# Performance work log

Hardware: AMD Instinct MI355X
Metric: run time of the kernel (lower is better)

Reference implementation:

```python
import jax, jax.numpy as jnp
import numpy as np

APREC = 8   # activation fractional bits
PPREC = 8   # parameter fractional bits
IWIDTH = 3  # integer width -> clamp to [-2**IWIDTH, 2**IWIDTH - 1]

QMAX = 2.0 ** IWIDTH - 1.0
QMIN = -(2.0 ** IWIDTH)


def quant(v, prec):
    # round to 2**-prec grid (torch.round and jnp.round both round-half-to-even)
    s = 2.0 ** prec
    return jnp.round(v * s) / s


def round_max(v):
    # the relu-chain in the source is exactly a clamp to [QMIN, QMAX]
    return jnp.clip(v, QMIN, QMAX)


def fixed_point_conv(x, w, b):
    """Quantized 'conv': each elementwise product w[j,m,p,q]*x[b,m,k+p,l+q] is
    rounded to the activation grid and clamped BEFORE summation, then bias added.
    x: [B,Cin,H,W], w: [Cout,Cin,K,K], b: [Cout].
    Loop is over the KxK fixed kernel offsets (25), fully vectorized over B/Cout/Cin/space."""
    w = quant(w, PPREC)
    b = quant(b, PPREC)
    K = w.shape[2]
    Ho = x.shape[2] - K + 1
    Wo = x.shape[3] - K + 1
    out = jnp.zeros((x.shape[0], w.shape[0], Ho, Wo), dtype=x.dtype)
    for p in range(K):
        for q in range(K):
            # [B, Cout, Cin, Ho, Wo]
            prod = x[:, None, :, p:p + Ho, q:q + Wo] * w[None, :, :, p, q, None, None]
            prod = round_max(quant(prod, APREC))
            out = out + prod.sum(axis=2)
    return out + b[None, :, None, None]


def fixed_point_fc(x, w, b):
    # x: [B, in], w: [out, in], b: [out]
    w = round_max(quant(w, PPREC))
    b = round_max(quant(b, PPREC))
    x = round_max(quant(x, APREC))
    out = x @ w.T + b[None, :]
    out = round_max(out)
    return quant(out, APREC)


def max_pool2(x):
    return jax.lax.reduce_window(x, -jnp.inf, jax.lax.max,
                                 (1, 1, 2, 2), (1, 1, 2, 2), 'VALID')


def setup_inputs() -> dict:
    key = jax.random.key(0)
    ks = jax.random.split(key, 9)
    B = 2048
    return {
        'x': jax.random.normal(ks[0], (B, 1, 28, 28), jnp.float32),
        'conv1_w': jax.random.normal(ks[1], (10, 1, 5, 5), jnp.float32) * 0.2,
        'conv1_b': jax.random.normal(ks[2], (10,), jnp.float32) * 0.1,
        'conv2_w': jax.random.normal(ks[3], (20, 10, 5, 5), jnp.float32) * 0.1,
        'conv2_b': jax.random.normal(ks[4], (20,), jnp.float32) * 0.1,
        'fc1_w': jax.random.normal(ks[5], (50, 320), jnp.float32) * 0.05,
        'fc1_b': jax.random.normal(ks[6], (50,), jnp.float32) * 0.05,
        'fc2_w': jax.random.normal(ks[7], (10, 50), jnp.float32) * 0.1,
        'fc2_b': jax.random.normal(ks[8], (10,), jnp.float32) * 0.1,
    }


def reference(x, conv1_w, conv1_b, conv2_w, conv2_b, fc1_w, fc1_b, fc2_w, fc2_b):
    x = quant(x, APREC)
    conv1_input = x
    x = fixed_point_conv(x, conv1_w, conv1_b)          # [B,10,24,24]
    x = quant(x, APREC)
    conv1_output = x
    x = jax.nn.relu(max_pool2(x))                      # [B,10,12,12]
    x = quant(x, APREC)
    conv2_input = x
    x = fixed_point_conv(x, conv2_w, conv2_b)          # [B,20,8,8]
    x = quant(x, APREC)
    conv2_output = x
    # Dropout2d / F.dropout are identity in eval mode
    x = jax.nn.relu(max_pool2(x))                      # [B,20,4,4]
    x = x.reshape(-1, 320)
    x = quant(x, APREC)
    fc1_input = x
    x = fixed_point_fc(x, fc1_w, fc1_b)                # [B,50]
    x = quant(x, APREC)
    fc1_output = x
    x = jax.nn.relu(x)
    x = quant(x, APREC)
    fc2_input = x
    x = fixed_point_fc(x, fc2_w, fc2_b)                # [B,10]
    x = quant(x, APREC)
    fc2_output = x
    logp = jax.nn.log_softmax(x, axis=1)
    return (logp, conv1_input, conv1_output, conv2_input, conv2_output,
            fc1_input, fc1_output, fc2_input, fc2_output)
```

## Files before the change

### kernel.cpp

```cpp
#include <hip/hip_runtime.h>
#include <math.h>


#define NB 2048

#define OFF_LOGP   0
#define OFF_C1IN   (OFF_LOGP  + NB*10)
#define OFF_C1OUT  (OFF_C1IN  + NB*784)
#define OFF_C2IN   (OFF_C1OUT + NB*5760)
#define OFF_C2OUT  (OFF_C2IN  + NB*1440)
#define OFF_FC1IN  (OFF_C2OUT + NB*1280)
#define OFF_FC1OUT (OFF_FC1IN + NB*320)
#define OFF_FC2IN  (OFF_FC1OUT+ NB*50)
#define OFF_FC2OUT (OFF_FC2IN + NB*50)

__device__ __forceinline__ float clamp8(float v) {
    return __builtin_amdgcn_fmed3f(v, -8.0f, 7.0f);
}

__global__ __launch_bounds__(256, 3)
void k1_conv1(const float* __restrict__ x,
              const float* __restrict__ cw1, const float* __restrict__ cb1,
              float* __restrict__ out)
{
    __shared__ float s_w1[125];
    __shared__ float s_b1[5];
    __shared__ __align__(16) float s_x[784];

    const int t    = threadIdx.x;
    const int img  = blockIdx.x >> 1;
    const int half = blockIdx.x & 1;

    if (t < 125) s_w1[t] = rintf(cw1[half * 125 + t] * 256.0f);
    if (t < 5)   s_b1[t] = rintf(cb1[half * 5 + t] * 256.0f);

    const float* xg = x + (size_t)img * 784;
    float* c1in_g = out + OFF_C1IN + (size_t)img * 784;
    for (int i = t; i < 784; i += 256) {
        float v = rintf(xg[i] * 256.0f) * (1.0f / 256.0f);
        s_x[i] = v;
        if (half == 0) c1in_g[i] = v;
    }
    __syncthreads();

    if (t < 240) {
        const int co_l = t / 48;
        const int co   = half * 5 + co_l;
        const int r    = t % 48;
        const int i    = r >> 1;
        const int jh   = r & 1;

        float acc[12];
        #pragma unroll
        for (int j = 0; j < 12; j++) acc[j] = 0.0f;

        #pragma unroll
        for (int p = 0; p < 5; p++) {
            float xr[16];
            const float* row = &s_x[(i + p) * 28 + 12 * jh];
            #pragma unroll
            for (int k = 0; k < 4; k++) {
                float4 v4 = *(const float4*)(row + 4 * k);
                xr[4*k] = v4.x; xr[4*k+1] = v4.y; xr[4*k+2] = v4.z; xr[4*k+3] = v4.w;
            }
            #pragma unroll
            for (int q = 0; q < 5; q++) {
                float w = s_w1[co_l * 25 + p * 5 + q];
                #pragma unroll
                for (int j = 0; j < 12; j++) {
                    acc[j] += rintf(xr[q + j] * w);
                }
            }
        }
        const float b = s_b1[co_l];
        float v[12];
        #pragma unroll
        for (int j = 0; j < 12; j++) v[j] = (acc[j] + b) * (1.0f / 256.0f);

        float* gdst = out + OFF_C1OUT + (size_t)img * 5760 + co * 576 + i * 24 + 12 * jh;
        #pragma unroll
        for (int k = 0; k < 3; k++) {
            float4 st = { v[4*k], v[4*k+1], v[4*k+2], v[4*k+3] };
            *(float4*)(gdst + 4 * k) = st;
        }

        float m[6];
        #pragma unroll
        for (int j2 = 0; j2 < 6; j2++) m[j2] = fmaxf(v[2*j2], v[2*j2+1]);
        float pm[6];
        #pragma unroll
        for (int j2 = 0; j2 < 6; j2++) pm[j2] = __shfl_xor(m[j2], 2);

        if ((i & 1) == 0) {
            float pr[6];
            #pragma unroll
            for (int j2 = 0; j2 < 6; j2++)
                pr[j2] = fmaxf(fmaxf(m[j2], pm[j2]), 0.0f);
            float* g = out + OFF_C2IN + (size_t)img * 1440 + co * 144 + (i >> 1) * 12 + 6 * jh;
            #pragma unroll
            for (int k = 0; k < 3; k++) {
                float2 st = { pr[2*k], pr[2*k+1] };
                *(float2*)(g + 2 * k) = st;
            }
        }
    }
}

__global__ __launch_bounds__(320, 2)
void k2_rest(const float* __restrict__ cw2, const float* __restrict__ cb2,
             const float* __restrict__ fw1, const float* __restrict__ fb1,
             const float* __restrict__ fw2, const float* __restrict__ fb2,
             float* __restrict__ out)
{
    __shared__ __align__(16) float s_w2[5600];
    __shared__ float s_b2[20];
    __shared__ __align__(16) float s_p1[1440];
    __shared__ float s_p2[320];
    __shared__ float s_fc2in[50];
    __shared__ float s_fc2out[10];

    const int t   = threadIdx.x;
    const int img = blockIdx.x;

    for (int idx = t; idx < 5000; idx += 320) {
        int cc = idx / 25, q = idx % 25;
        s_w2[cc * 28 + q] = rintf(cw2[idx] * 256.0f);
    }
    if (t < 20) s_b2[t] = rintf(cb2[t] * 256.0f);

    const float* p1g = out + OFF_C2IN + (size_t)img * 1440;
    for (int i = t; i < 1440; i += 320) s_p1[i] = p1g[i];
    __syncthreads();

    const int co = t >> 4;
    const int i  = (t >> 1) & 7;
    const int jh = t & 1;

    float acc[4] = {0.f, 0.f, 0.f, 0.f};
    for (int ci = 0; ci < 10; ci++) {
        float wr_[28];
        const float* wb = s_w2 + (co * 10 + ci) * 28;
        #pragma unroll
        for (int k = 0; k < 7; k++) {
            float4 v4 = *(const float4*)(wb + 4 * k);
            wr_[4*k] = v4.x; wr_[4*k+1] = v4.y; wr_[4*k+2] = v4.z; wr_[4*k+3] = v4.w;
        }
        const float* xb = s_p1 + ci * 144 + jh * 4;
        #pragma unroll
        for (int p = 0; p < 5; p++) {
            const float* row = xb + (i + p) * 12;
            float4 a4 = *(const float4*)(row);
            float4 b4 = *(const float4*)(row + 4);
            float xr[8] = { a4.x, a4.y, a4.z, a4.w, b4.x, b4.y, b4.z, b4.w };
            #pragma unroll
            for (int q = 0; q < 5; q++) {
                float w = wr_[p * 5 + q];
                #pragma unroll
                for (int j = 0; j < 4; j++) {
                    acc[j] += rintf(xr[q + j] * w);
                }
            }
        }
    }
    const float b2 = s_b2[co];
    float v[4];
    #pragma unroll
    for (int j = 0; j < 4; j++) v[j] = (acc[j] + b2) * (1.0f / 256.0f);

    {
        float4 st = { v[0], v[1], v[2], v[3] };
        *(float4*)(out + OFF_C2OUT + (size_t)img * 1280 + co * 64 + i * 8 + jh * 4) = st;
    }

    float m0 = fmaxf(v[0], v[1]);
    float m1 = fmaxf(v[2], v[3]);
    float pm0 = __shfl_xor(m0, 2);
    float pm1 = __shfl_xor(m1, 2);
    if ((i & 1) == 0) {
        float r0 = fmaxf(fmaxf(m0, pm0), 0.0f);
        float r1 = fmaxf(fmaxf(m1, pm1), 0.0f);
        int o = co * 16 + (i >> 1) * 4 + jh * 2;
        out[OFF_FC1IN + (size_t)img * 320 + o]     = r0;
        out[OFF_FC1IN + (size_t)img * 320 + o + 1] = r1;
        s_p2[o]     = clamp8(r0);
        s_p2[o + 1] = clamp8(r1);
    }
    __syncthreads();

    float* s_fcp = s_p1;
    if (t < 250) {
        const int j = t / 5, c = t % 5;
        const float* wr = fw1 + j * 320 + c * 64;
        const float* xr = s_p2 + c * 64;
        float s = 0.0f;
        #pragma unroll 8
        for (int k = 0; k < 64; k++) {
            float wq = clamp8(rintf(wr[k] * 256.0f) * (1.0f / 256.0f));
            s = fmaf(xr[k], wq, s);
        }
        s_fcp[t] = s;
    }
    __syncthreads();

    if (t < 50) {
        float acc1 = clamp8(rintf(fb1[t] * 256.0f) * (1.0f / 256.0f));
        #pragma unroll
        for (int c = 0; c < 5; c++) acc1 += s_fcp[t * 5 + c];
        float o1 = rintf(clamp8(acc1) * 256.0f) * (1.0f / 256.0f);
        out[OFF_FC1OUT + (size_t)img * 50 + t] = o1;
        float r = fmaxf(o1, 0.0f);
        out[OFF_FC2IN + (size_t)img * 50 + t] = r;
        s_fc2in[t] = clamp8(r);
    }
    __syncthreads();

    if (t < 10) {
        float acc2 = clamp8(rintf(fb2[t] * 256.0f) * (1.0f / 256.0f));
        const float* wr = fw2 + t * 50;
        for (int k = 0; k < 50; k++) {
            float wq = clamp8(rintf(wr[k] * 256.0f) * (1.0f / 256.0f));
            acc2 = fmaf(s_fc2in[k], wq, acc2);
        }
        float o2 = rintf(clamp8(acc2) * 256.0f) * (1.0f / 256.0f);
        out[OFF_FC2OUT + (size_t)img * 10 + t] = o2;
        s_fc2out[t] = o2;
    }
    __syncthreads();

    if (t == 0) {
        float m = s_fc2out[0];
        for (int k = 1; k < 10; k++) m = fmaxf(m, s_fc2out[k]);
        float ssum = 0.0f;
        for (int k = 0; k < 10; k++) ssum += expf(s_fc2out[k] - m);
        float lse = m + logf(ssum);
        for (int k = 0; k < 10; k++)
            out[OFF_LOGP + (size_t)img * 10 + k] = s_fc2out[k] - lse;
    }
}

extern "C" void kernel_launch(void* const* d_in, const int* in_sizes, int n_in,
                              void* d_out, int out_size, void* d_ws, size_t ws_size,
                              hipStream_t stream) {
    const float* x   = (const float*)d_in[0];
    const float* cw1 = (const float*)d_in[1];
    const float* cb1 = (const float*)d_in[2];
    const float* cw2 = (const float*)d_in[3];
    const float* cb2 = (const float*)d_in[4];
    const float* fw1 = (const float*)d_in[5];
    const float* fb1 = (const float*)d_in[6];
    const float* fw2 = (const float*)d_in[7];
    const float* fb2 = (const float*)d_in[8];
    float* o = (float*)d_out;

    k1_conv1<<<2 * NB, 256, 0, stream>>>(x, cw1, cb1, o);
    k2_rest <<<NB, 320, 0, stream>>>(cw2, cb2, fw1, fb1, fw2, fb2, o);
}
```

Before: 191.7 us.

## Fuse conv1 and rest into one kernel processing four images per block

Merges the two kernels into a single kernel in which each 320-thread block handles four images. Conv1 results stay in LDS for conv2, so the global round-trip of the pooled activations disappears, and the conv2 weights are loaded once per four images instead of once per image. Conv2 is re-tiled so each thread computes a 4x4 output patch with register-cached inputs, and the fc1 weights are read as float4. In exchange the grid has only 512 blocks with about 59KB of LDS each, which reduces occupancy and parallelism.

```diff
diff --git a/kernel.cpp b/kernel.cpp
--- a/kernel.cpp
+++ b/kernel.cpp
@@ -14,41 +14,73 @@
 #define OFF_FC2IN  (OFF_FC1OUT+ NB*50)
 #define OFF_FC2OUT (OFF_FC2IN + NB*50)
 
+#define W1_OFF  0
+#define B1_OFF  280
+#define B2_OFF  290
+#define W2_OFF  312
+#define X_OFF   5912
+#define P1_OFF  9048
+#define LDS_FLOATS 14808
+#define P2_OFF   X_OFF
+#define FC2IN_OFF (X_OFF + 1280)
+#define FC2OUT_OFF (X_OFF + 1488)
+
 __device__ __forceinline__ float clamp8(float v) {
     return __builtin_amdgcn_fmed3f(v, -8.0f, 7.0f);
 }
 
-__global__ __launch_bounds__(256, 3)
-void k1_conv1(const float* __restrict__ x,
-              const float* __restrict__ cw1, const float* __restrict__ cb1,
-              float* __restrict__ out)
+__global__ __launch_bounds__(320, 2)
+void net_fused(const float* __restrict__ x,
+               const float* __restrict__ cw1, const float* __restrict__ cb1,
+               const float* __restrict__ cw2, const float* __restrict__ cb2,
+               const float* __restrict__ fw1, const float* __restrict__ fb1,
+               const float* __restrict__ fw2, const float* __restrict__ fb2,
+               float* __restrict__ out)
 {
-    __shared__ float s_w1[125];
-    __shared__ float s_b1[5];
-    __shared__ __align__(16) float s_x[784];
+    __shared__ __align__(16) float lds[LDS_FLOATS];
 
     const int t    = threadIdx.x;
-    const int img  = blockIdx.x >> 1;
-    const int half = blockIdx.x & 1;
-
-    if (t < 125) s_w1[t] = rintf(cw1[half * 125 + t] * 256.0f);
-    if (t < 5)   s_b1[t] = rintf(cb1[half * 5 + t] * 256.0f);
-
-    const float* xg = x + (size_t)img * 784;
-    float* c1in_g = out + OFF_C1IN + (size_t)img * 784;
-    for (int i = t; i < 784; i += 256) {
-        float v = rintf(xg[i] * 256.0f) * (1.0f / 256.0f);
-        s_x[i] = v;
-        if (half == 0) c1in_g[i] = v;
-    }
-    __syncthreads();
-
-    if (t < 240) {
-        const int co_l = t / 48;
-        const int co   = half * 5 + co_l;
-        const int r    = t % 48;
-        const int i    = r >> 1;
-        const int jh   = r & 1;
+    const int img0 = blockIdx.x * 4;
+
+    if (t < 250) lds[W1_OFF + (t / 25) * 28 + (t % 25)] = rintf(cw1[t] * 256.0f);
+    if (t < 10)  lds[B1_OFF + t] = rintf(cb1[t] * 256.0f);
+    if (t < 20)  lds[B2_OFF + t] = rintf(cb2[t] * 256.0f);
+    for (int f = t; f < 5000; f += 320) {
+        int cc = f / 25, q = f % 25;
+        lds[W2_OFF + cc * 28 + q] = rintf(cw2[f] * 256.0f);
+    }
+
+    {
+        const float* xg = x + (size_t)img0 * 784;
+        float* g = out + OFF_C1IN + (size_t)img0 * 784;
+        for (int f = t; f < 3136; f += 320) {
+            float v = rintf(xg[f] * 256.0f) * (1.0f / 256.0f);
+            lds[X_OFF + f] = v;
+            g[f] = v;
+        }
+    }
+    __syncthreads();
+
+    #pragma unroll 1
+    for (int iter = 0; iter < 6; iter++) {
+        const int T     = iter * 320 + t;
+        const int img_l = T / 480;
+        const int rem   = T % 480;
+        const int co    = rem / 48;
+        const int r     = rem % 48;
+        const int i     = r >> 1;
+        const int jh    = r & 1;
+        const int img   = img0 + img_l;
+
+        float wreg[28];
+        {
+            const float* wb = lds + W1_OFF + co * 28;
+            #pragma unroll
+            for (int k = 0; k < 7; k++) {
+                float4 v4 = *(const float4*)(wb + 4 * k);
+                wreg[4*k] = v4.x; wreg[4*k+1] = v4.y; wreg[4*k+2] = v4.z; wreg[4*k+3] = v4.w;
+            }
+        }
 
         float acc[12];
         #pragma unroll
@@ -57,7 +89,7 @@
         #pragma unroll
         for (int p = 0; p < 5; p++) {
             float xr[16];
-            const float* row = &s_x[(i + p) * 28 + 12 * jh];
+            const float* row = lds + X_OFF + img_l * 784 + (i + p) * 28 + 12 * jh;
             #pragma unroll
             for (int k = 0; k < 4; k++) {
                 float4 v4 = *(const float4*)(row + 4 * k);
@@ -65,14 +97,13 @@
             }
             #pragma unroll
             for (int q = 0; q < 5; q++) {
-                float w = s_w1[co_l * 25 + p * 5 + q];
+                float w = wreg[p * 5 + q];
                 #pragma unroll
-                for (int j = 0; j < 12; j++) {
+                for (int j = 0; j < 12; j++)
                     acc[j] += rintf(xr[q + j] * w);
-                }
-            }
-        }
-        const float b = s_b1[co_l];
+            }
+        }
+        const float b = lds[B1_OFF + co];
         float v[12];
         #pragma unroll
         for (int j = 0; j < 12; j++) v[j] = (acc[j] + b) * (1.0f / 256.0f);
@@ -96,145 +127,158 @@
             #pragma unroll
             for (int j2 = 0; j2 < 6; j2++)
                 pr[j2] = fmaxf(fmaxf(m[j2], pm[j2]), 0.0f);
-            float* g = out + OFF_C2IN + (size_t)img * 1440 + co * 144 + (i >> 1) * 12 + 6 * jh;
+            const int o = co * 144 + (i >> 1) * 12 + 6 * jh;
+            float* g = out + OFF_C2IN + (size_t)img * 1440 + o;
+            float* s = lds + P1_OFF + img_l * 1440 + o;
             #pragma unroll
             for (int k = 0; k < 3; k++) {
                 float2 st = { pr[2*k], pr[2*k+1] };
                 *(float2*)(g + 2 * k) = st;
-            }
-        }
-    }
-}
-
-__global__ __launch_bounds__(320, 2)
-void k2_rest(const float* __restrict__ cw2, const float* __restrict__ cb2,
-             const float* __restrict__ fw1, const float* __restrict__ fb1,
-             const float* __restrict__ fw2, const float* __restrict__ fb2,
-             float* __restrict__ out)
-{
-    __shared__ __align__(16) float s_w2[5600];
-    __shared__ float s_b2[20];
-    __shared__ __align__(16) float s_p1[1440];
-    __shared__ float s_p2[320];
-    __shared__ float s_fc2in[50];
-    __shared__ float s_fc2out[10];
-
-    const int t   = threadIdx.x;
-    const int img = blockIdx.x;
-
-    for (int idx = t; idx < 5000; idx += 320) {
-        int cc = idx / 25, q = idx % 25;
-        s_w2[cc * 28 + q] = rintf(cw2[idx] * 256.0f);
-    }
-    if (t < 20) s_b2[t] = rintf(cb2[t] * 256.0f);
-
-    const float* p1g = out + OFF_C2IN + (size_t)img * 1440;
-    for (int i = t; i < 1440; i += 320) s_p1[i] = p1g[i];
-    __syncthreads();
-
-    const int co = t >> 4;
-    const int i  = (t >> 1) & 7;
-    const int jh = t & 1;
-
-    float acc[4] = {0.f, 0.f, 0.f, 0.f};
-    for (int ci = 0; ci < 10; ci++) {
-        float wr_[28];
-        const float* wb = s_w2 + (co * 10 + ci) * 28;
-        #pragma unroll
-        for (int k = 0; k < 7; k++) {
-            float4 v4 = *(const float4*)(wb + 4 * k);
-            wr_[4*k] = v4.x; wr_[4*k+1] = v4.y; wr_[4*k+2] = v4.z; wr_[4*k+3] = v4.w;
-        }
-        const float* xb = s_p1 + ci * 144 + jh * 4;
-        #pragma unroll
-        for (int p = 0; p < 5; p++) {
-            const float* row = xb + (i + p) * 12;
-            float4 a4 = *(const float4*)(row);
-            float4 b4 = *(const float4*)(row + 4);
-            float xr[8] = { a4.x, a4.y, a4.z, a4.w, b4.x, b4.y, b4.z, b4.w };
-            #pragma unroll
-            for (int q = 0; q < 5; q++) {
-                float w = wr_[p * 5 + q];
+                s[2*k] = pr[2*k]; s[2*k+1] = pr[2*k+1];
+            }
+        }
+    }
+    __syncthreads();
+
+    {
+        const int img_l = t / 80;
+        const int rt    = t % 80;
+        const int co    = rt >> 2;
+        const int ih    = (rt >> 1) & 1;
+        const int jh    = rt & 1;
+        const int img   = img0 + img_l;
+
+        float acc[16];
+        #pragma unroll
+        for (int j = 0; j < 16; j++) acc[j] = 0.0f;
+
+        const float* wbase  = lds + W2_OFF + co * 280;
+        const float* xibase = lds + P1_OFF + img_l * 1440 + jh * 4;
+        #pragma unroll 1
+        for (int ci = 0; ci < 10; ci++) {
+            float wreg[28];
+            {
+                const float* wb = wbase + ci * 28;
                 #pragma unroll
-                for (int j = 0; j < 4; j++) {
-                    acc[j] += rintf(xr[q + j] * w);
+                for (int k = 0; k < 7; k++) {
+                    float4 v4 = *(const float4*)(wb + 4 * k);
+                    wreg[4*k] = v4.x; wreg[4*k+1] = v4.y; wreg[4*k+2] = v4.z; wreg[4*k+3] = v4.w;
                 }
             }
-        }
-    }
-    const float b2 = s_b2[co];
-    float v[4];
-    #pragma unroll
-    for (int j = 0; j < 4; j++) v[j] = (acc[j] + b2) * (1.0f / 256.0f);
-
-    {
-        float4 st = { v[0], v[1], v[2], v[3] };
-        *(float4*)(out + OFF_C2OUT + (size_t)img * 1280 + co * 64 + i * 8 + jh * 4) = st;
-    }
-
-    float m0 = fmaxf(v[0], v[1]);
-    float m1 = fmaxf(v[2], v[3]);
-    float pm0 = __shfl_xor(m0, 2);
-    float pm1 = __shfl_xor(m1, 2);
-    if ((i & 1) == 0) {
-        float r0 = fmaxf(fmaxf(m0, pm0), 0.0f);
-        float r1 = fmaxf(fmaxf(m1, pm1), 0.0f);
-        int o = co * 16 + (i >> 1) * 4 + jh * 2;
-        out[OFF_FC1IN + (size_t)img * 320 + o]     = r0;
-        out[OFF_FC1IN + (size_t)img * 320 + o + 1] = r1;
-        s_p2[o]     = clamp8(r0);
-        s_p2[o + 1] = clamp8(r1);
-    }
-    __syncthreads();
-
-    float* s_fcp = s_p1;
-    if (t < 250) {
-        const int j = t / 5, c = t % 5;
+            float xr[64];
+            const float* xb = xibase + ci * 144 + ih * 48;
+            #pragma unroll
+            for (int rr = 0; rr < 8; rr++) {
+                float4 a4 = *(const float4*)(xb + rr * 12);
+                float4 b4 = *(const float4*)(xb + rr * 12 + 4);
+                xr[rr*8+0] = a4.x; xr[rr*8+1] = a4.y; xr[rr*8+2] = a4.z; xr[rr*8+3] = a4.w;
+                xr[rr*8+4] = b4.x; xr[rr*8+5] = b4.y; xr[rr*8+6] = b4.z; xr[rr*8+7] = b4.w;
+            }
+            #pragma unroll
+            for (int p = 0; p < 5; p++) {
+                #pragma unroll
+                for (int q = 0; q < 5; q++) {
+                    float w = wreg[p * 5 + q];
+                    #pragma unroll
+                    for (int rr = 0; rr < 4; rr++) {
+                        #pragma unroll
+                        for (int cc = 0; cc < 4; cc++)
+                            acc[rr*4+cc] += rintf(xr[(rr+p)*8 + q + cc] * w);
+                    }
+                }
+            }
+        }
+        const float b2 = lds[B2_OFF + co];
+        float v[16];
+        #pragma unroll
+        for (int j = 0; j < 16; j++) v[j] = (acc[j] + b2) * (1.0f / 256.0f);
+
+        float* gdst = out + OFF_C2OUT + (size_t)img * 1280 + co * 64 + ih * 32 + jh * 4;
+        #pragma unroll
+        for (int rr = 0; rr < 4; rr++) {
+            float4 st = { v[rr*4+0], v[rr*4+1], v[rr*4+2], v[rr*4+3] };
+            *(float4*)(gdst + rr * 8) = st;
+        }
+
+        #pragma unroll
+        for (int a = 0; a < 2; a++) {
+            #pragma unroll
+            for (int bb = 0; bb < 2; bb++) {
+                float pm = fmaxf(fmaxf(v[(2*a)*4 + 2*bb], v[(2*a)*4 + 2*bb + 1]),
+                                 fmaxf(v[(2*a+1)*4 + 2*bb], v[(2*a+1)*4 + 2*bb + 1]));
+                pm = fmaxf(pm, 0.0f);
+                const int o = co * 16 + (ih * 2 + a) * 4 + (jh * 2 + bb);
+                out[OFF_FC1IN + (size_t)img * 320 + o] = pm;
+                lds[P2_OFF + img_l * 320 + o] = clamp8(pm);
+            }
+        }
+    }
+    __syncthreads();
+
+    float* s_fcp = lds + P1_OFF;
+    #pragma unroll 1
+    for (int T = t; T < 1000; T += 320) {
+        const int img_l = T / 250;
+        const int rem   = T % 250;
+        const int j     = rem / 5;
+        const int c     = rem % 5;
         const float* wr = fw1 + j * 320 + c * 64;
-        const float* xr = s_p2 + c * 64;
+        const float* xr = lds + P2_OFF + img_l * 320 + c * 64;
         float s = 0.0f;
-        #pragma unroll 8
-        for (int k = 0; k < 64; k++) {
-            float wq = clamp8(rintf(wr[k] * 256.0f) * (1.0f / 256.0f));
-            s = fmaf(xr[k], wq, s);
-        }
-        s_fcp[t] = s;
-    }
-    __syncthreads();
-
-    if (t < 50) {
-        float acc1 = clamp8(rintf(fb1[t] * 256.0f) * (1.0f / 256.0f));
-        #pragma unroll
-        for (int c = 0; c < 5; c++) acc1 += s_fcp[t * 5 + c];
+        #pragma unroll
+        for (int k4 = 0; k4 < 16; k4++) {
+            float4 w4 = *(const float4*)(wr + 4 * k4);
+            s = fmaf(xr[4*k4+0], clamp8(rintf(w4.x * 256.0f) * (1.0f / 256.0f)), s);
+            s = fmaf(xr[4*k4+1], clamp8(rintf(w4.y * 256.0f) * (1.0f / 256.0f)), s);
+            s = fmaf(xr[4*k4+2], clamp8(rintf(w4.z * 256.0f) * (1.0f / 256.0f)), s);
+            s = fmaf(xr[4*k4+3], clamp8(rintf(w4.w * 256.0f) * (1.0f / 256.0f)), s);
+        }
+        s_fcp[T] = s;
+    }
+    __syncthreads();
+
+    if (t < 200) {
+        const int img_l = t / 50;
+        const int j     = t % 50;
+        const int img   = img0 + img_l;
+        float acc1 = clamp8(rintf(fb1[j] * 256.0f) * (1.0f / 256.0f));
+        #pragma unroll
+        for (int c = 0; c < 5; c++) acc1 += s_fcp[img_l * 250 + j * 5 + c];
         float o1 = rintf(clamp8(acc1) * 256.0f) * (1.0f / 256.0f);
-        out[OFF_FC1OUT + (size_t)img * 50 + t] = o1;
+        out[OFF_FC1OUT + (size_t)img * 50 + j] = o1;
         float r = fmaxf(o1, 0.0f);
-        out[OFF_FC2IN + (size_t)img * 50 + t] = r;
-        s_fc2in[t] = clamp8(r);
-    }
-    __syncthreads();
-
-    if (t < 10) {
-        float acc2 = clamp8(rintf(fb2[t] * 256.0f) * (1.0f / 256.0f));
-        const float* wr = fw2 + t * 50;
+        out[OFF_FC2IN + (size_t)img * 50 + j] = r;
+        lds[FC2IN_OFF + img_l * 52 + j] = clamp8(r);
+    }
+    __syncthreads();
+
+    if (t < 40) {
+        const int img_l = t / 10;
+        const int j     = t % 10;
+        const int img   = img0 + img_l;
+        float acc2 = clamp8(rintf(fb2[j] * 256.0f) * (1.0f / 256.0f));
+        const float* wr = fw2 + j * 50;
+        const float* xr = lds + FC2IN_OFF + img_l * 52;
         for (int k = 0; k < 50; k++) {
             float wq = clamp8(rintf(wr[k] * 256.0f) * (1.0f / 256.0f));
-            acc2 = fmaf(s_fc2in[k], wq, acc2);
+            acc2 = fmaf(xr[k], wq, acc2);
         }
         float o2 = rintf(clamp8(acc2) * 256.0f) * (1.0f / 256.0f);
-        out[OFF_FC2OUT + (size_t)img * 10 + t] = o2;
-        s_fc2out[t] = o2;
-    }
-    __syncthreads();
-
-    if (t == 0) {
-        float m = s_fc2out[0];
-        for (int k = 1; k < 10; k++) m = fmaxf(m, s_fc2out[k]);
+        out[OFF_FC2OUT + (size_t)img * 10 + j] = o2;
+        lds[FC2OUT_OFF + img_l * 10 + j] = o2;
+    }
+    __syncthreads();
+
+    if (t < 4) {
+        const int img = img0 + t;
+        const float* s = lds + FC2OUT_OFF + t * 10;
+        float m = s[0];
+        for (int k = 1; k < 10; k++) m = fmaxf(m, s[k]);
         float ssum = 0.0f;
-        for (int k = 0; k < 10; k++) ssum += expf(s_fc2out[k] - m);
+        for (int k = 0; k < 10; k++) ssum += expf(s[k] - m);
         float lse = m + logf(ssum);
         for (int k = 0; k < 10; k++)
-            out[OFF_LOGP + (size_t)img * 10 + k] = s_fc2out[k] - lse;
+            out[OFF_LOGP + (size_t)img * 10 + k] = s[k] - lse;
     }
 }
 
@@ -252,6 +296,6 @@
     const float* fb2 = (const float*)d_in[8];
     float* o = (float*)d_out;
 
-    k1_conv1<<<2 * NB, 256, 0, stream>>>(x, cw1, cb1, o);
-    k2_rest <<<NB, 320, 0, stream>>>(cw2, cb2, fw1, fb1, fw2, fb2, o);
+    net_fused<<<NB / 4, 320, 0, stream>>>(x, cw1, cb1, cw2, cb2,
+                                          fw1, fb1, fw2, fb2, o);
 }
```

Result: slower. 226.1 us (+18.0%).

## Process two images per k2 block with two output rows per thread

Applied to the files above, without the earlier changes.

The second kernel now handles two images per block, so the conv2 weight load and requantisation from global into shared memory is paid once per two images. Each thread computes two adjacent output rows and reuses the shared input row between them, which lets the 2x2 max-pool happen inside the thread without shuffles. FC1 weights are read as float4, and the FC stages loop over both images. The trade is half as many blocks, more shared memory per block, and serial FC tails that now cover two images.

```diff
diff --git a/kernel.cpp b/kernel.cpp
--- a/kernel.cpp
+++ b/kernel.cpp
@@ -67,9 +67,8 @@
             for (int q = 0; q < 5; q++) {
                 float w = s_w1[co_l * 25 + p * 5 + q];
                 #pragma unroll
-                for (int j = 0; j < 12; j++) {
+                for (int j = 0; j < 12; j++)
                     acc[j] += rintf(xr[q + j] * w);
-                }
             }
         }
         const float b = s_b1[co_l];
@@ -114,127 +113,170 @@
 {
     __shared__ __align__(16) float s_w2[5600];
     __shared__ float s_b2[20];
-    __shared__ __align__(16) float s_p1[1440];
-    __shared__ float s_p2[320];
-    __shared__ float s_fc2in[50];
-    __shared__ float s_fc2out[10];
-
-    const int t   = threadIdx.x;
-    const int img = blockIdx.x;
-
-    for (int idx = t; idx < 5000; idx += 320) {
-        int cc = idx / 25, q = idx % 25;
-        s_w2[cc * 28 + q] = rintf(cw2[idx] * 256.0f);
+    __shared__ __align__(16) float s_p1[2880];
+    __shared__ float s_p2[640];
+    __shared__ float s_fc2in[104];
+    __shared__ float s_fc2out[20];
+
+    const int t    = threadIdx.x;
+    const int img0 = blockIdx.x * 2;
+
+    for (int f = t; f < 5000; f += 320) {
+        int cc = f / 25, q = f % 25;
+        s_w2[cc * 28 + q] = rintf(cw2[f] * 256.0f);
     }
     if (t < 20) s_b2[t] = rintf(cb2[t] * 256.0f);
 
-    const float* p1g = out + OFF_C2IN + (size_t)img * 1440;
-    for (int i = t; i < 1440; i += 320) s_p1[i] = p1g[i];
-    __syncthreads();
-
-    const int co = t >> 4;
-    const int i  = (t >> 1) & 7;
-    const int jh = t & 1;
-
-    float acc[4] = {0.f, 0.f, 0.f, 0.f};
+    {
+        const float4* p1g = (const float4*)(out + OFF_C2IN + (size_t)img0 * 1440);
+        float4* p1s = (float4*)s_p1;
+        for (int f = t; f < 720; f += 320) p1s[f] = p1g[f];
+    }
+    __syncthreads();
+
+    const int img_l = t / 160;
+    const int rt    = t % 160;
+    const int co    = rt >> 3;
+    const int i2    = (rt >> 1) & 3;
+    const int jh    = rt & 1;
+    const int img   = img0 + img_l;
+
+    float acc[8];
+    #pragma unroll
+    for (int j = 0; j < 8; j++) acc[j] = 0.0f;
+
+    const float* wb0 = s_w2 + co * 280;
+    const float* xb0 = s_p1 + img_l * 1440 + jh * 4 + i2 * 24;
+    #pragma unroll 1
     for (int ci = 0; ci < 10; ci++) {
-        float wr_[28];
-        const float* wb = s_w2 + (co * 10 + ci) * 28;
-        #pragma unroll
-        for (int k = 0; k < 7; k++) {
-            float4 v4 = *(const float4*)(wb + 4 * k);
-            wr_[4*k] = v4.x; wr_[4*k+1] = v4.y; wr_[4*k+2] = v4.z; wr_[4*k+3] = v4.w;
-        }
-        const float* xb = s_p1 + ci * 144 + jh * 4;
+        float wreg[28];
+        {
+            const float* wb = wb0 + ci * 28;
+            #pragma unroll
+            for (int k = 0; k < 7; k++) {
+                float4 v4 = *(const float4*)(wb + 4 * k);
+                wreg[4*k] = v4.x; wreg[4*k+1] = v4.y; wreg[4*k+2] = v4.z; wreg[4*k+3] = v4.w;
+            }
+        }
+        const float* xb = xb0 + ci * 144;
+        float ra[8];
+        {
+            float4 a4 = *(const float4*)(xb);
+            float4 b4 = *(const float4*)(xb + 4);
+            ra[0]=a4.x; ra[1]=a4.y; ra[2]=a4.z; ra[3]=a4.w;
+            ra[4]=b4.x; ra[5]=b4.y; ra[6]=b4.z; ra[7]=b4.w;
+        }
         #pragma unroll
         for (int p = 0; p < 5; p++) {
-            const float* row = xb + (i + p) * 12;
-            float4 a4 = *(const float4*)(row);
-            float4 b4 = *(const float4*)(row + 4);
-            float xr[8] = { a4.x, a4.y, a4.z, a4.w, b4.x, b4.y, b4.z, b4.w };
+            float rb[8];
+            {
+                const float* rp = xb + (p + 1) * 12;
+                float4 a4 = *(const float4*)(rp);
+                float4 b4 = *(const float4*)(rp + 4);
+                rb[0]=a4.x; rb[1]=a4.y; rb[2]=a4.z; rb[3]=a4.w;
+                rb[4]=b4.x; rb[5]=b4.y; rb[6]=b4.z; rb[7]=b4.w;
+            }
             #pragma unroll
             for (int q = 0; q < 5; q++) {
-                float w = wr_[p * 5 + q];
+                float w = wreg[p * 5 + q];
                 #pragma unroll
-                for (int j = 0; j < 4; j++) {
-                    acc[j] += rintf(xr[q + j] * w);
-                }
-            }
+                for (int cc = 0; cc < 4; cc++)
+                    acc[cc]     += rintf(ra[q + cc] * w);
+                #pragma unroll
+                for (int cc = 0; cc < 4; cc++)
+                    acc[4 + cc] += rintf(rb[q + cc] * w);
+            }
+            #pragma unroll
+            for (int z = 0; z < 8; z++) ra[z] = rb[z];
         }
     }
     const float b2 = s_b2[co];
-    float v[4];
+    float v[8];
     #pragma unroll
-    for (int j = 0; j < 4; j++) v[j] = (acc[j] + b2) * (1.0f / 256.0f);
+    for (int j = 0; j < 8; j++) v[j] = (acc[j] + b2) * (1.0f / 256.0f);
 
     {
-        float4 st = { v[0], v[1], v[2], v[3] };
-        *(float4*)(out + OFF_C2OUT + (size_t)img * 1280 + co * 64 + i * 8 + jh * 4) = st;
-    }
-
-    float m0 = fmaxf(v[0], v[1]);
-    float m1 = fmaxf(v[2], v[3]);
-    float pm0 = __shfl_xor(m0, 2);
-    float pm1 = __shfl_xor(m1, 2);
-    if ((i & 1) == 0) {
-        float r0 = fmaxf(fmaxf(m0, pm0), 0.0f);
-        float r1 = fmaxf(fmaxf(m1, pm1), 0.0f);
-        int o = co * 16 + (i >> 1) * 4 + jh * 2;
-        out[OFF_FC1IN + (size_t)img * 320 + o]     = r0;
-        out[OFF_FC1IN + (size_t)img * 320 + o + 1] = r1;
-        s_p2[o]     = clamp8(r0);
-        s_p2[o + 1] = clamp8(r1);
+        float* gdst = out + OFF_C2OUT + (size_t)img * 1280 + co * 64 + (2 * i2) * 8 + jh * 4;
+        float4 st0 = { v[0], v[1], v[2], v[3] };
+        float4 st1 = { v[4], v[5], v[6], v[7] };
+        *(float4*)(gdst)     = st0;
+        *(float4*)(gdst + 8) = st1;
+    }
+
+    {
+        float p0 = fmaxf(fmaxf(v[0], v[1]), fmaxf(v[4], v[5]));
+        float p1 = fmaxf(fmaxf(v[2], v[3]), fmaxf(v[6], v[7]));
+        p0 = fmaxf(p0, 0.0f);
+        p1 = fmaxf(p1, 0.0f);
+        const int o = co * 16 + i2 * 4 + 2 * jh;
+        float2 st = { p0, p1 };
+        *(float2*)(out + OFF_FC1IN + (size_t)img * 320 + o) = st;
+        s_p2[img_l * 320 + o]     = clamp8(p0);
+        s_p2[img_l * 320 + o + 1] = clamp8(p1);
     }
     __syncthreads();
 
     float* s_fcp = s_p1;
-    if (t < 250) {
-        const int j = t / 5, c = t % 5;
+    #pragma unroll 1
+    for (int T = t; T < 500; T += 320) {
+        const int il  = T / 250;
+        const int rem = T % 250;
+        const int j   = rem / 5;
+        const int c   = rem % 5;
         const float* wr = fw1 + j * 320 + c * 64;
-        const float* xr = s_p2 + c * 64;
+        const float* xr = s_p2 + il * 320 + c * 64;
         float s = 0.0f;
-        #pragma unroll 8
-        for (int k = 0; k < 64; k++) {
-            float wq = clamp8(rintf(wr[k] * 256.0f) * (1.0f / 256.0f));
-            s = fmaf(xr[k], wq, s);
-        }
-        s_fcp[t] = s;
-    }
-    __syncthreads();
-
-    if (t < 50) {
-        float acc1 = clamp8(rintf(fb1[t] * 256.0f) * (1.0f / 256.0f));
-        #pragma unroll
-        for (int c = 0; c < 5; c++) acc1 += s_fcp[t * 5 + c];
+        #pragma unroll
+        for (int k4 = 0; k4 < 16; k4++) {
+            float4 w4 = *(const float4*)(wr + 4 * k4);
+            s = fmaf(xr[4*k4+0], clamp8(rintf(w4.x * 256.0f) * (1.0f / 256.0f)), s);
+            s = fmaf(xr[4*k4+1], clamp8(rintf(w4.y * 256.0f) * (1.0f / 256.0f)), s);
+            s = fmaf(xr[4*k4+2], clamp8(rintf(w4.z * 256.0f) * (1.0f / 256.0f)), s);
+            s = fmaf(xr[4*k4+3], clamp8(rintf(w4.w * 256.0f) * (1.0f / 256.0f)), s);
+        }
+        s_fcp[T] = s;
+    }
+    __syncthreads();
+
+    if (t < 100) {
+        const int il = t / 50;
+        const int j  = t % 50;
+        float acc1 = clamp8(rintf(fb1[j] * 256.0f) * (1.0f / 256.0f));
+        #pragma unroll
+        for (int c = 0; c < 5; c++) acc1 += s_fcp[il * 250 + j * 5 + c];
         float o1 = rintf(clamp8(acc1) * 256.0f) * (1.0f / 256.0f);
-        out[OFF_FC1OUT + (size_t)img * 50 + t] = o1;
+        out[OFF_FC1OUT + (size_t)(img0 + il) * 50 + j] = o1;
         float r = fmaxf(o1, 0.0f);
-        out[OFF_FC2IN + (size_t)img * 50 + t] = r;
-        s_fc2in[t] = clamp8(r);
-    }
-    __syncthreads();
-
-    if (t < 10) {
-        float acc2 = clamp8(rintf(fb2[t] * 256.0f) * (1.0f / 256.0f));
-        const float* wr = fw2 + t * 50;
+        out[OFF_FC2IN + (size_t)(img0 + il) * 50 + j] = r;
+        s_fc2in[il * 52 + j] = clamp8(r);
+    }
+    __syncthreads();
+
+    if (t < 20) {
+        const int il = t / 10;
+        const int j  = t % 10;
+        float acc2 = clamp8(rintf(fb2[j] * 256.0f) * (1.0f / 256.0f));
+        const float* wr = fw2 + j * 50;
+        const float* xr = s_fc2in + il * 52;
         for (int k = 0; k < 50; k++) {
             float wq = clamp8(rintf(wr[k] * 256.0f) * (1.0f / 256.0f));
-            acc2 = fmaf(s_fc2in[k], wq, acc2);
+            acc2 = fmaf(xr[k], wq, acc2);
         }
         float o2 = rintf(clamp8(acc2) * 256.0f) * (1.0f / 256.0f);
-        out[OFF_FC2OUT + (size_t)img * 10 + t] = o2;
-        s_fc2out[t] = o2;
-    }
-    __syncthreads();
-
-    if (t == 0) {
-        float m = s_fc2out[0];
-        for (int k = 1; k < 10; k++) m = fmaxf(m, s_fc2out[k]);
+        out[OFF_FC2OUT + (size_t)(img0 + il) * 10 + j] = o2;
+        s_fc2out[il * 10 + j] = o2;
+    }
+    __syncthreads();
+
+    if (t < 2) {
+        const float* s = s_fc2out + t * 10;
+        float m = s[0];
+        for (int k = 1; k < 10; k++) m = fmaxf(m, s[k]);
         float ssum = 0.0f;
-        for (int k = 0; k < 10; k++) ssum += expf(s_fc2out[k] - m);
+        for (int k = 0; k < 10; k++) ssum += expf(s[k] - m);
         float lse = m + logf(ssum);
         for (int k = 0; k < 10; k++)
-            out[OFF_LOGP + (size_t)img * 10 + k] = s_fc2out[k] - lse;
+            out[OFF_LOGP + (size_t)(img0 + t) * 10 + k] = s[k] - lse;
     }
 }
 
@@ -253,5 +295,5 @@
     float* o = (float*)d_out;
 
     k1_conv1<<<2 * NB, 256, 0, stream>>>(x, cw1, cb1, o);
-    k2_rest <<<NB, 320, 0, stream>>>(cw2, cb2, fw1, fb1, fw2, fb2, o);
-}
+    k2_rest <<<NB / 2, 320, 0, stream>>>(cw2, cb2, fw1, fb1, fw2, fb2, o);
+}
```

Measured after the change: 219.8 us. 14.7% more time.

## Fuse conv1 and remaining network into one kernel per image

Applied to the files above, without the earlier changes.

Merges the conv1 kernel into the second kernel so each block computes the whole network for one image, keeping the pooled conv1 output in shared memory instead of rereading it from global memory. This removes one launch and the global round trip of the conv2 input. It also vectorizes the fc1 weight loads. The trade-off is that conv1 now runs on 320 threads in two passes per image instead of 512 threads across two blocks, so each block does more serial work.

```diff
diff --git a/kernel.cpp b/kernel.cpp
--- a/kernel.cpp
+++ b/kernel.cpp
@@ -14,189 +14,203 @@
 #define OFF_FC2IN  (OFF_FC1OUT+ NB*50)
 #define OFF_FC2OUT (OFF_FC2IN + NB*50)
 
+#define W1_OFF   0
+#define B1_OFF   280
+#define B2_OFF   290
+#define W2_OFF   312
+#define X_OFF    5912
+#define P1_OFF   6696
+#define P2_OFF   8136
+#define FC2IN_OFF  8456
+#define FC2OUT_OFF 8508
+#define LDS_FLOATS 8520
+
 __device__ __forceinline__ float clamp8(float v) {
     return __builtin_amdgcn_fmed3f(v, -8.0f, 7.0f);
 }
 
-__global__ __launch_bounds__(256, 3)
-void k1_conv1(const float* __restrict__ x,
-              const float* __restrict__ cw1, const float* __restrict__ cb1,
-              float* __restrict__ out)
-{
-    __shared__ float s_w1[125];
-    __shared__ float s_b1[5];
-    __shared__ __align__(16) float s_x[784];
-
-    const int t    = threadIdx.x;
-    const int img  = blockIdx.x >> 1;
-    const int half = blockIdx.x & 1;
-
-    if (t < 125) s_w1[t] = rintf(cw1[half * 125 + t] * 256.0f);
-    if (t < 5)   s_b1[t] = rintf(cb1[half * 5 + t] * 256.0f);
-
-    const float* xg = x + (size_t)img * 784;
-    float* c1in_g = out + OFF_C1IN + (size_t)img * 784;
-    for (int i = t; i < 784; i += 256) {
-        float v = rintf(xg[i] * 256.0f) * (1.0f / 256.0f);
-        s_x[i] = v;
-        if (half == 0) c1in_g[i] = v;
-    }
-    __syncthreads();
-
-    if (t < 240) {
-        const int co_l = t / 48;
-        const int co   = half * 5 + co_l;
-        const int r    = t % 48;
-        const int i    = r >> 1;
-        const int jh   = r & 1;
-
-        float acc[12];
-        #pragma unroll
-        for (int j = 0; j < 12; j++) acc[j] = 0.0f;
-
-        #pragma unroll
-        for (int p = 0; p < 5; p++) {
-            float xr[16];
-            const float* row = &s_x[(i + p) * 28 + 12 * jh];
-            #pragma unroll
-            for (int k = 0; k < 4; k++) {
-                float4 v4 = *(const float4*)(row + 4 * k);
-                xr[4*k] = v4.x; xr[4*k+1] = v4.y; xr[4*k+2] = v4.z; xr[4*k+3] = v4.w;
-            }
-            #pragma unroll
-            for (int q = 0; q < 5; q++) {
-                float w = s_w1[co_l * 25 + p * 5 + q];
-                #pragma unroll
-                for (int j = 0; j < 12; j++) {
-                    acc[j] += rintf(xr[q + j] * w);
-                }
-            }
-        }
-        const float b = s_b1[co_l];
-        float v[12];
-        #pragma unroll
-        for (int j = 0; j < 12; j++) v[j] = (acc[j] + b) * (1.0f / 256.0f);
-
-        float* gdst = out + OFF_C1OUT + (size_t)img * 5760 + co * 576 + i * 24 + 12 * jh;
-        #pragma unroll
-        for (int k = 0; k < 3; k++) {
-            float4 st = { v[4*k], v[4*k+1], v[4*k+2], v[4*k+3] };
-            *(float4*)(gdst + 4 * k) = st;
-        }
-
-        float m[6];
-        #pragma unroll
-        for (int j2 = 0; j2 < 6; j2++) m[j2] = fmaxf(v[2*j2], v[2*j2+1]);
-        float pm[6];
-        #pragma unroll
-        for (int j2 = 0; j2 < 6; j2++) pm[j2] = __shfl_xor(m[j2], 2);
-
-        if ((i & 1) == 0) {
-            float pr[6];
-            #pragma unroll
-            for (int j2 = 0; j2 < 6; j2++)
-                pr[j2] = fmaxf(fmaxf(m[j2], pm[j2]), 0.0f);
-            float* g = out + OFF_C2IN + (size_t)img * 1440 + co * 144 + (i >> 1) * 12 + 6 * jh;
-            #pragma unroll
-            for (int k = 0; k < 3; k++) {
-                float2 st = { pr[2*k], pr[2*k+1] };
-                *(float2*)(g + 2 * k) = st;
-            }
-        }
-    }
-}
-
 __global__ __launch_bounds__(320, 2)
-void k2_rest(const float* __restrict__ cw2, const float* __restrict__ cb2,
+void net_one(const float* __restrict__ x,
+             const float* __restrict__ cw1, const float* __restrict__ cb1,
+             const float* __restrict__ cw2, const float* __restrict__ cb2,
              const float* __restrict__ fw1, const float* __restrict__ fb1,
              const float* __restrict__ fw2, const float* __restrict__ fb2,
              float* __restrict__ out)
 {
-    __shared__ __align__(16) float s_w2[5600];
-    __shared__ float s_b2[20];
-    __shared__ __align__(16) float s_p1[1440];
-    __shared__ float s_p2[320];
-    __shared__ float s_fc2in[50];
-    __shared__ float s_fc2out[10];
+    __shared__ __align__(16) float lds[LDS_FLOATS];
 
     const int t   = threadIdx.x;
     const int img = blockIdx.x;
 
-    for (int idx = t; idx < 5000; idx += 320) {
-        int cc = idx / 25, q = idx % 25;
-        s_w2[cc * 28 + q] = rintf(cw2[idx] * 256.0f);
-    }
-    if (t < 20) s_b2[t] = rintf(cb2[t] * 256.0f);
-
-    const float* p1g = out + OFF_C2IN + (size_t)img * 1440;
-    for (int i = t; i < 1440; i += 320) s_p1[i] = p1g[i];
-    __syncthreads();
-
-    const int co = t >> 4;
-    const int i  = (t >> 1) & 7;
-    const int jh = t & 1;
-
-    float acc[4] = {0.f, 0.f, 0.f, 0.f};
-    for (int ci = 0; ci < 10; ci++) {
-        float wr_[28];
-        const float* wb = s_w2 + (co * 10 + ci) * 28;
+    if (t < 250) lds[W1_OFF + (t / 25) * 28 + (t % 25)] = rintf(cw1[t] * 256.0f);
+    if (t < 10)  lds[B1_OFF + t] = rintf(cb1[t] * 256.0f);
+    if (t < 20)  lds[B2_OFF + t] = rintf(cb2[t] * 256.0f);
+    for (int f = t; f < 5000; f += 320) {
+        int cc = f / 25, q = f % 25;
+        lds[W2_OFF + cc * 28 + q] = rintf(cw2[f] * 256.0f);
+    }
+
+    {
+        const float* xg = x + (size_t)img * 784;
+        float* g = out + OFF_C1IN + (size_t)img * 784;
+        for (int f = t; f < 784; f += 320) {
+            float v = rintf(xg[f] * 256.0f) * (1.0f / 256.0f);
+            lds[X_OFF + f] = v;
+            g[f] = v;
+        }
+    }
+    __syncthreads();
+
+    #pragma unroll 1
+    for (int iter = 0; iter < 2; iter++) {
+        const int T = iter * 320 + t;
+        if (T < 480) {
+            const int co = T / 48;
+            const int r  = T % 48;
+            const int i  = r >> 1;
+            const int jh = r & 1;
+
+            float wreg[28];
+            {
+                const float* wb = lds + W1_OFF + co * 28;
+                #pragma unroll
+                for (int k = 0; k < 7; k++) {
+                    float4 v4 = *(const float4*)(wb + 4 * k);
+                    wreg[4*k] = v4.x; wreg[4*k+1] = v4.y; wreg[4*k+2] = v4.z; wreg[4*k+3] = v4.w;
+                }
+            }
+
+            float acc[12];
+            #pragma unroll
+            for (int j = 0; j < 12; j++) acc[j] = 0.0f;
+
+            #pragma unroll
+            for (int p = 0; p < 5; p++) {
+                float xr[16];
+                const float* row = lds + X_OFF + (i + p) * 28 + 12 * jh;
+                #pragma unroll
+                for (int k = 0; k < 4; k++) {
+                    float4 v4 = *(const float4*)(row + 4 * k);
+                    xr[4*k] = v4.x; xr[4*k+1] = v4.y; xr[4*k+2] = v4.z; xr[4*k+3] = v4.w;
+                }
+                #pragma unroll
+                for (int q = 0; q < 5; q++) {
+                    float w = wreg[p * 5 + q];
+                    #pragma unroll
+                    for (int j = 0; j < 12; j++)
+                        acc[j] += rintf(xr[q + j] * w);
+                }
+            }
+            const float b = lds[B1_OFF + co];
+            float v[12];
+            #pragma unroll
+            for (int j = 0; j < 12; j++) v[j] = (acc[j] + b) * (1.0f / 256.0f);
+
+            float* gdst = out + OFF_C1OUT + (size_t)img * 5760 + co * 576 + i * 24 + 12 * jh;
+            #pragma unroll
+            for (int k = 0; k < 3; k++) {
+                float4 st = { v[4*k], v[4*k+1], v[4*k+2], v[4*k+3] };
+                *(float4*)(gdst + 4 * k) = st;
+            }
+
+            float m[6];
+            #pragma unroll
+            for (int j2 = 0; j2 < 6; j2++) m[j2] = fmaxf(v[2*j2], v[2*j2+1]);
+            float pm[6];
+            #pragma unroll
+            for (int j2 = 0; j2 < 6; j2++) pm[j2] = __shfl_xor(m[j2], 2);
+
+            if ((i & 1) == 0) {
+                float pr[6];
+                #pragma unroll
+                for (int j2 = 0; j2 < 6; j2++)
+                    pr[j2] = fmaxf(fmaxf(m[j2], pm[j2]), 0.0f);
+                const int o = co * 144 + (i >> 1) * 12 + 6 * jh;
+                float* g = out + OFF_C2IN + (size_t)img * 1440 + o;
+                float* s = lds + P1_OFF + o;
+                #pragma unroll
+                for (int k = 0; k < 3; k++) {
+                    float2 st = { pr[2*k], pr[2*k+1] };
+                    *(float2*)(g + 2 * k) = st;
+                    s[2*k] = pr[2*k]; s[2*k+1] = pr[2*k+1];
+                }
+            }
+        }
+    }
+    __syncthreads();
+
+    {
+        const int co = t >> 4;
+        const int i  = (t >> 1) & 7;
+        const int jh = t & 1;
+
+        float acc[4] = {0.f, 0.f, 0.f, 0.f};
+        #pragma unroll 1
+        for (int ci = 0; ci < 10; ci++) {
+            float wreg[28];
+            {
+                const float* wb = lds + W2_OFF + (co * 10 + ci) * 28;
+                #pragma unroll
+                for (int k = 0; k < 7; k++) {
+                    float4 v4 = *(const float4*)(wb + 4 * k);
+                    wreg[4*k] = v4.x; wreg[4*k+1] = v4.y; wreg[4*k+2] = v4.z; wreg[4*k+3] = v4.w;
+                }
+            }
+            const float* xb = lds + P1_OFF + ci * 144 + jh * 4;
+            #pragma unroll
+            for (int p = 0; p < 5; p++) {
+                const float* row = xb + (i + p) * 12;
+                float4 a4 = *(const float4*)(row);
+                float4 b4 = *(const float4*)(row + 4);
+                float xr[8] = { a4.x, a4.y, a4.z, a4.w, b4.x, b4.y, b4.z, b4.w };
+                #pragma unroll
+                for (int q = 0; q < 5; q++) {
+                    float w = wreg[p * 5 + q];
+                    #pragma unroll
+                    for (int j = 0; j < 4; j++)
+                        acc[j] += rintf(xr[q + j] * w);
+                }
+            }
+        }
+        const float b2 = lds[B2_OFF + co];
+        float v[4];
         #pragma unroll
-        for (int k = 0; k < 7; k++) {
-            float4 v4 = *(const float4*)(wb + 4 * k);
-            wr_[4*k] = v4.x; wr_[4*k+1] = v4.y; wr_[4*k+2] = v4.z; wr_[4*k+3] = v4.w;
-        }
-        const float* xb = s_p1 + ci * 144 + jh * 4;
-        #pragma unroll
-        for (int p = 0; p < 5; p++) {
-            const float* row = xb + (i + p) * 12;
-            float4 a4 = *(const float4*)(row);
-            float4 b4 = *(const float4*)(row + 4);
-            float xr[8] = { a4.x, a4.y, a4.z, a4.w, b4.x, b4.y, b4.z, b4.w };
-            #pragma unroll
-            for (int q = 0; q < 5; q++) {
-                float w = wr_[p * 5 + q];
-                #pragma unroll
-                for (int j = 0; j < 4; j++) {
-                    acc[j] += rintf(xr[q + j] * w);
-                }
-            }
-        }
-    }
-    const float b2 = s_b2[co];
-    float v[4];
-    #pragma unroll
-    for (int j = 0; j < 4; j++) v[j] = (acc[j] + b2) * (1.0f / 256.0f);
-
-    {
-        float4 st = { v[0], v[1], v[2], v[3] };
-        *(float4*)(out + OFF_C2OUT + (size_t)img * 1280 + co * 64 + i * 8 + jh * 4) = st;
-    }
-
-    float m0 = fmaxf(v[0], v[1]);
-    float m1 = fmaxf(v[2], v[3]);
-    float pm0 = __shfl_xor(m0, 2);
-    float pm1 = __shfl_xor(m1, 2);
-    if ((i & 1) == 0) {
-        float r0 = fmaxf(fmaxf(m0, pm0), 0.0f);
-        float r1 = fmaxf(fmaxf(m1, pm1), 0.0f);
-        int o = co * 16 + (i >> 1) * 4 + jh * 2;
-        out[OFF_FC1IN + (size_t)img * 320 + o]     = r0;
-        out[OFF_FC1IN + (size_t)img * 320 + o + 1] = r1;
-        s_p2[o]     = clamp8(r0);
-        s_p2[o + 1] = clamp8(r1);
-    }
-    __syncthreads();
-
-    float* s_fcp = s_p1;
+        for (int j = 0; j < 4; j++) v[j] = (acc[j] + b2) * (1.0f / 256.0f);
+
+        {
+            float4 st = { v[0], v[1], v[2], v[3] };
+            *(float4*)(out + OFF_C2OUT + (size_t)img * 1280 + co * 64 + i * 8 + jh * 4) = st;
+        }
+
+        float m0 = fmaxf(v[0], v[1]);
+        float m1 = fmaxf(v[2], v[3]);
+        float pm0 = __shfl_xor(m0, 2);
+        float pm1 = __shfl_xor(m1, 2);
+        if ((i & 1) == 0) {
+            float r0 = fmaxf(fmaxf(m0, pm0), 0.0f);
+            float r1 = fmaxf(fmaxf(m1, pm1), 0.0f);
+            const int o = co * 16 + (i >> 1) * 4 + jh * 2;
+            float2 st = { r0, r1 };
+            *(float2*)(out + OFF_FC1IN + (size_t)img * 320 + o) = st;
+            lds[P2_OFF + o]     = clamp8(r0);
+            lds[P2_OFF + o + 1] = clamp8(r1);
+        }
+    }
+    __syncthreads();
+
+    float* s_fcp = lds + P1_OFF;
     if (t < 250) {
         const int j = t / 5, c = t % 5;
         const float* wr = fw1 + j * 320 + c * 64;
-        const float* xr = s_p2 + c * 64;
+        const float* xr = lds + P2_OFF + c * 64;
         float s = 0.0f;
-        #pragma unroll 8
-        for (int k = 0; k < 64; k++) {
-            float wq = clamp8(rintf(wr[k] * 256.0f) * (1.0f / 256.0f));
-            s = fmaf(xr[k], wq, s);
+        #pragma unroll
+        for (int k4 = 0; k4 < 16; k4++) {
+            float4 w4 = *(const float4*)(wr + 4 * k4);
+            s = fmaf(xr[4*k4+0], clamp8(rintf(w4.x * 256.0f) * (1.0f / 256.0f)), s);
+            s = fmaf(xr[4*k4+1], clamp8(rintf(w4.y * 256.0f) * (1.0f / 256.0f)), s);
+            s = fmaf(xr[4*k4+2], clamp8(rintf(w4.z * 256.0f) * (1.0f / 256.0f)), s);
+            s = fmaf(xr[4*k4+3], clamp8(rintf(w4.w * 256.0f) * (1.0f / 256.0f)), s);
         }
         s_fcp[t] = s;
     }
@@ -210,31 +224,33 @@
         out[OFF_FC1OUT + (size_t)img * 50 + t] = o1;
         float r = fmaxf(o1, 0.0f);
         out[OFF_FC2IN + (size_t)img * 50 + t] = r;
-        s_fc2in[t] = clamp8(r);
+        lds[FC2IN_OFF + t] = clamp8(r);
     }
     __syncthreads();
 
     if (t < 10) {
         float acc2 = clamp8(rintf(fb2[t] * 256.0f) * (1.0f / 256.0f));
         const float* wr = fw2 + t * 50;
+        const float* xr = lds + FC2IN_OFF;
         for (int k = 0; k < 50; k++) {
             float wq = clamp8(rintf(wr[k] * 256.0f) * (1.0f / 256.0f));
-            acc2 = fmaf(s_fc2in[k], wq, acc2);
+            acc2 = fmaf(xr[k], wq, acc2);
         }
         float o2 = rintf(clamp8(acc2) * 256.0f) * (1.0f / 256.0f);
         out[OFF_FC2OUT + (size_t)img * 10 + t] = o2;
-        s_fc2out[t] = o2;
+        lds[FC2OUT_OFF + t] = o2;
     }
     __syncthreads();
 
     if (t == 0) {
-        float m = s_fc2out[0];
-        for (int k = 1; k < 10; k++) m = fmaxf(m, s_fc2out[k]);
+        const float* s = lds + FC2OUT_OFF;
+        float m = s[0];
+        for (int k = 1; k < 10; k++) m = fmaxf(m, s[k]);
         float ssum = 0.0f;
-        for (int k = 0; k < 10; k++) ssum += expf(s_fc2out[k] - m);
+        for (int k = 0; k < 10; k++) ssum += expf(s[k] - m);
         float lse = m + logf(ssum);
         for (int k = 0; k < 10; k++)
-            out[OFF_LOGP + (size_t)img * 10 + k] = s_fc2out[k] - lse;
+            out[OFF_LOGP + (size_t)img * 10 + k] = s[k] - lse;
     }
 }
 
@@ -252,6 +268,6 @@
     const float* fb2 = (const float*)d_in[8];
     float* o = (float*)d_out;
 
-    k1_conv1<<<2 * NB, 256, 0, stream>>>(x, cw1, cb1, o);
-    k2_rest <<<NB, 320, 0, stream>>>(cw2, cb2, fw1, fb1, fw2, fb2, o);
+    net_one<<<NB, 320, 0, stream>>>(x, cw1, cb1, cw2, cb2,
+                                    fw1, fb1, fw2, fb2, o);
 }
```

Result: slower. 253.6 us (+32.3%).
